# Performance work log

Measured on AMD Instinct MI355X. Metric: run time of the kernel, lower is better.

The kernel has to match this reference:

```python
import jax, jax.numpy as jnp
import numpy as np

N_NODES = 100000
N_EDGES = 1600000
HIDDEN = 128
N_LAYERS = 4
EPS = 0.0  # GINConv default eps, train_eps=False


def setup_inputs() -> dict:
    key = jax.random.key(0)
    ks = jax.random.split(key, 6)
    scale = 1.0 / np.sqrt(HIDDEN)
    return {
        "x": jax.random.normal(ks[0], (N_NODES, HIDDEN), dtype=jnp.float32),
        "edge_index": jax.random.randint(ks[1], (2, N_EDGES), 0, N_NODES, dtype=jnp.int64),
        "W1": jax.random.normal(ks[2], (N_LAYERS, HIDDEN, HIDDEN), dtype=jnp.float32) * scale,
        "b1": jnp.zeros((N_LAYERS, HIDDEN), dtype=jnp.float32),
        "W2": jax.random.normal(ks[3], (N_LAYERS, HIDDEN, HIDDEN), dtype=jnp.float32) * scale,
        "b2": jnp.zeros((N_LAYERS, HIDDEN), dtype=jnp.float32),
    }


def reference(x, edge_index, W1, b1, W2, b2):
    src = edge_index[0]  # message sources (x_j)
    dst = edge_index[1]  # aggregation targets
    n = x.shape[0]
    for l in range(N_LAYERS):
        x_in = x
        # scatter-add aggregation: sum_{j in N(i)} x_j
        agg = jax.ops.segment_sum(x[src], dst, num_segments=n)
        out = agg + (1.0 + EPS) * x
        # GIN MLP: Linear -> ReLU -> Linear
        h = jax.nn.relu(out @ W1[l] + b1[l]) @ W2[l] + b2[l]
        # outer loop: relu, dropout (identity in eval), residual
        x = x_in + jax.nn.relu(h)
    return x
```

## Files before the change

### kernel.cpp

```cpp
#include <hip/hip_runtime.h>

typedef unsigned short u16;
typedef unsigned int u32;

constexpr int NN = 100000;
constexpr int NE = 1600000;
constexpr int H = 128;

constexpr int NB = 196;
constexpr int BCAP = 10240;
constexpr int PB_E = 4096;
constexpr int PB_BLOCKS = (NE + PB_E - 1) / PB_E;

typedef __bf16 bf16x8 __attribute__((ext_vector_type(8)));
typedef float f32x16 __attribute__((ext_vector_type(16)));

__device__ __forceinline__ u16 f2bf(float f) {
    union { float f; u32 u; } cv; cv.f = f;
    u32 r = (cv.u + 0x7fffu + ((cv.u >> 16) & 1u)) >> 16;
    return (u16)r;
}
__device__ __forceinline__ float bflo(u32 u) {
    union { u32 u; float f; } cv; cv.u = u << 16; return cv.f;
}
__device__ __forceinline__ float bfhi(u32 u) {
    union { u32 u; float f; } cv; cv.u = u & 0xffff0000u; return cv.f;
}

__global__ void detect_kernel(const int* __restrict__ e, int* __restrict__ flag,
                              int* __restrict__ gcursor) {
    __shared__ int anynz;
    if (threadIdx.x == 0) anynz = 0;
    __syncthreads();
    int local = 0;
    for (int i = threadIdx.x; i < 4096; i += 256)
        if (e[2 * i + 1] != 0) local = 1;
    if (local) atomicOr(&anynz, 1);
    __syncthreads();
    if (threadIdx.x == 0) flag[0] = anynz ? 1 : 2;
    if (threadIdx.x < NB) gcursor[threadIdx.x] = 0;
}

__global__ __launch_bounds__(256) void part_kernel(const int* __restrict__ e,
                                                   const int* __restrict__ flag,
                                                   int* __restrict__ gcursor,
                                                   u32* __restrict__ ebuf) {
    __shared__ int lcnt[NB];
    __shared__ int gbaseL[NB];
    const int t = threadIdx.x;
    if (t < NB) lcnt[t] = 0;
    __syncthreads();
    const int st = flag[0];
    const int base = blockIdx.x * PB_E;
    u32 pk[16]; int bk[16]; int rk[16];
#pragma unroll
    for (int j = 0; j < 16; ++j) {
        int i = base + j * 256 + t;
        bk[j] = -1;
        if (i < NE) {
            int s = e[st * i];
            int d = e[st * (NE + i)];
            int b = d >> 9;
            pk[j] = (u32)s | ((u32)(d & 511) << 17);
            bk[j] = b;
            rk[j] = atomicAdd(&lcnt[b], 1);
        }
    }
    __syncthreads();
    if (t < NB) gbaseL[t] = atomicAdd(&gcursor[t], lcnt[t]);
    __syncthreads();
#pragma unroll
    for (int j = 0; j < 16; ++j)
        if (bk[j] >= 0)
            ebuf[bk[j] * BCAP + gbaseL[bk[j]] + rk[j]] = pk[j];
}

__global__ __launch_bounds__(256) void bscan_kernel(const int* __restrict__ gcursor,
                                                    int* __restrict__ bbase,
                                                    int* __restrict__ offs) {
    __shared__ int s[256];
    int t = threadIdx.x;
    int v = (t < NB) ? gcursor[t] : 0;
    s[t] = v;
    __syncthreads();
    for (int off = 1; off < 256; off <<= 1) {
        int u = (t >= off) ? s[t - off] : 0;
        __syncthreads();
        s[t] += u;
        __syncthreads();
    }
    if (t < NB) bbase[t] = s[t] - v;
    if (t == 0) offs[NN] = NE;
}

__global__ __launch_bounds__(256) void bfill_kernel(const u32* __restrict__ ebuf,
                                                    const int* __restrict__ gcursor,
                                                    const int* __restrict__ bbase,
                                                    int* __restrict__ offs,
                                                    int* __restrict__ colv) {
    __shared__ int ncnt[512];
    __shared__ int cur[512];
    __shared__ int ps[256];
    const int b = blockIdx.x, t = threadIdx.x;
    const int En = gcursor[b];
    const int bb = bbase[b];
    ncnt[t] = 0; ncnt[t + 256] = 0;
    __syncthreads();
    const u32* eb = ebuf + b * BCAP;
    for (int i = t; i < En; i += 256)
        atomicAdd(&ncnt[eb[i] >> 17], 1);
    __syncthreads();
    int s2 = ncnt[2 * t] + ncnt[2 * t + 1];
    ps[t] = s2;
    __syncthreads();
    for (int off = 1; off < 256; off <<= 1) {
        int u = (t >= off) ? ps[t - off] : 0;
        __syncthreads();
        ps[t] += u;
        __syncthreads();
    }
    int e0 = ps[t] - s2;
    cur[2 * t] = e0;
    cur[2 * t + 1] = e0 + ncnt[2 * t];
    __syncthreads();
    const int n0 = b * 512;
    for (int i = t; i < 512; i += 256)
        if (n0 + i < NN) offs[n0 + i] = bb + cur[i];
    __syncthreads();
    for (int i = t; i < En; i += 256) {
        u32 p = eb[i];
        int pos = atomicAdd(&cur[p >> 17], 1);
        colv[bb + pos] = (int)(p & 0x1FFFFu);
    }
}

__global__ void wtconv_kernel(const float* __restrict__ W1,
                              const float* __restrict__ W2,
                              u16* __restrict__ wt) {
    int t = blockIdx.x * 256 + threadIdx.x;
    int w = t >> 14;
    int r = t & 16383;
    int k = r >> 7, n = r & 127;
    int l = w >> 1, s = w & 1;
    const float* src = (s == 0 ? W1 : W2) + l * 16384;
    wt[w * 16384 + n * 128 + k] = f2bf(src[k * 128 + n]);
}

__global__ void xinit_kernel(const float* __restrict__ xin,
                             float* __restrict__ x, u16* __restrict__ xb) {
    int i = blockIdx.x * 256 + threadIdx.x;
    float4 v = ((const float4*)xin)[i];
    ((float4*)x)[i] = v;
    uint2 p;
    p.x = (u32)f2bf(v.x) | ((u32)f2bf(v.y) << 16);
    p.y = (u32)f2bf(v.z) | ((u32)f2bf(v.w) << 16);
    ((uint2*)xb)[i] = p;
}

__global__ __launch_bounds__(256) void agg_kernel(const u16* __restrict__ xb,
                                                  const int* __restrict__ colv,
                                                  const int* __restrict__ offs,
                                                  u16* __restrict__ out) {
    const int lane = threadIdx.x & 63;
    const int node = __builtin_amdgcn_readfirstlane(blockIdx.x * 4 + (threadIdx.x >> 6));
    const int rs = __builtin_amdgcn_readfirstlane(offs[node]);
    const int re = __builtin_amdgcn_readfirstlane(offs[node + 1]);
    u32 su = *(const u32*)(xb + node * H + lane * 2);
    float a0 = bflo(su), a1 = bfhi(su);
    for (int j = rs; j < re; j += 16) {
        int sidx[16];
#pragma unroll
        for (int q = 0; q < 16; ++q) {
            int idx = j + q;
            idx = idx < re ? idx : re - 1;
            sidx[q] = __builtin_amdgcn_readfirstlane(colv[idx]);
        }
        u32 uu[16];
#pragma unroll
        for (int q = 0; q < 16; ++q)
            uu[q] = *(const u32*)(xb + sidx[q] * H + lane * 2);
#pragma unroll
        for (int q = 0; q < 16; ++q) {
            u32 m = (j + q < re) ? 0xffffffffu : 0u;
            u32 u = uu[q] & m;
            a0 += bflo(u); a1 += bfhi(u);
        }
    }
    u32 o = (u32)f2bf(a0) | ((u32)f2bf(a1) << 16);
    *(u32*)(out + node * H + lane * 2) = o;
}

__global__ __launch_bounds__(256) void mlp_kernel(const u16* __restrict__ agg,
                                                  const u16* __restrict__ wt1,
                                                  const u16* __restrict__ wt2,
                                                  const float* __restrict__ b1,
                                                  const float* __restrict__ b2,
                                                  float* __restrict__ x,
                                                  u16* __restrict__ xb) {
    __shared__ u16 lds[128 * 128];
    const int tid = threadIdx.x;
    const int wave = tid >> 6, lane = tid & 63;
    const int wm = wave >> 1, wn = wave & 1;
    const int ml = lane & 31, g = lane >> 5;
    const int row0 = blockIdx.x * 128;

#pragma unroll
    for (int i = 0; i < 8; ++i) {
        int ch = tid + 256 * i;
        int r = ch >> 4, c = ch & 15;
        int4 v = make_int4(0, 0, 0, 0);
        int gr = row0 + r;
        if (gr < NN) v = *(const int4*)(agg + gr * H + c * 8);
        *(int4*)(&lds[r * H + ((c ^ (r & 15)) << 3)]) = v;
    }

    bf16x8 bfrag[2][8];
#pragma unroll
    for (int nt = 0; nt < 2; ++nt)
#pragma unroll
        for (int ks = 0; ks < 8; ++ks)
            bfrag[nt][ks] = *(const bf16x8*)(wt1 + (wn * 64 + nt * 32 + ml) * H + ks * 16 + g * 8);

    float bias1[2], bias2[2];
#pragma unroll
    for (int nt = 0; nt < 2; ++nt) {
        bias1[nt] = b1[wn * 64 + nt * 32 + ml];
        bias2[nt] = b2[wn * 64 + nt * 32 + ml];
    }

    __syncthreads();

    f32x16 acc[2][2];
#pragma unroll
    for (int mt = 0; mt < 2; ++mt)
#pragma unroll
        for (int nt = 0; nt < 2; ++nt)
#pragma unroll
            for (int i = 0; i < 16; ++i) acc[mt][nt][i] = 0.f;

#pragma unroll
    for (int ks = 0; ks < 8; ++ks) {
        bf16x8 afrag[2];
#pragma unroll
        for (int mt = 0; mt < 2; ++mt) {
            int m = wm * 64 + mt * 32 + ml;
            int chunk = (2 * ks + g) ^ (m & 15);
            afrag[mt] = *(const bf16x8*)(&lds[m * H + (chunk << 3)]);
        }
#pragma unroll
        for (int mt = 0; mt < 2; ++mt)
#pragma unroll
            for (int nt = 0; nt < 2; ++nt)
                acc[mt][nt] = __builtin_amdgcn_mfma_f32_32x32x16_bf16(
                    afrag[mt], bfrag[nt][ks], acc[mt][nt], 0, 0, 0);
    }

    __syncthreads();

#pragma unroll
    for (int mt = 0; mt < 2; ++mt)
#pragma unroll
        for (int nt = 0; nt < 2; ++nt)
#pragma unroll
            for (int reg = 0; reg < 16; ++reg) {
                int rm = wm * 64 + mt * 32 + (reg & 3) + ((reg >> 2) << 3) + 4 * g;
                int cn = wn * 64 + nt * 32 + ml;
                float v = acc[mt][nt][reg] + bias1[nt];
                v = v > 0.f ? v : 0.f;
                lds[rm * H + ((((cn >> 3) ^ (rm & 15))) << 3) + (cn & 7)] = f2bf(v);
            }

#pragma unroll
    for (int nt = 0; nt < 2; ++nt)
#pragma unroll
        for (int ks = 0; ks < 8; ++ks)
            bfrag[nt][ks] = *(const bf16x8*)(wt2 + (wn * 64 + nt * 32 + ml) * H + ks * 16 + g * 8);

#pragma unroll
    for (int mt = 0; mt < 2; ++mt)
#pragma unroll
        for (int nt = 0; nt < 2; ++nt)
#pragma unroll
            for (int i = 0; i < 16; ++i) acc[mt][nt][i] = 0.f;

    __syncthreads();

#pragma unroll
    for (int ks = 0; ks < 8; ++ks) {
        bf16x8 afrag[2];
#pragma unroll
        for (int mt = 0; mt < 2; ++mt) {
            int m = wm * 64 + mt * 32 + ml;
            int chunk = (2 * ks + g) ^ (m & 15);
            afrag[mt] = *(const bf16x8*)(&lds[m * H + (chunk << 3)]);
        }
#pragma unroll
        for (int mt = 0; mt < 2; ++mt)
#pragma unroll
            for (int nt = 0; nt < 2; ++nt)
                acc[mt][nt] = __builtin_amdgcn_mfma_f32_32x32x16_bf16(
                    afrag[mt], bfrag[nt][ks], acc[mt][nt], 0, 0, 0);
    }

    __syncthreads();

#pragma unroll
    for (int mt = 0; mt < 2; ++mt)
#pragma unroll
        for (int nt = 0; nt < 2; ++nt)
#pragma unroll
            for (int reg = 0; reg < 16; ++reg) {
                int rm = wm * 64 + mt * 32 + (reg & 3) + ((reg >> 2) << 3) + 4 * g;
                int cn = wn * 64 + nt * 32 + ml;
                float v = acc[mt][nt][reg] + bias2[nt];
                v = v > 0.f ? v : 0.f;
                lds[rm * H + ((((cn >> 3) ^ (rm & 15))) << 3) + (cn & 7)] = f2bf(v);
            }

    __syncthreads();

#pragma unroll
    for (int i = 0; i < 8; ++i) {
        int ch = tid + 256 * i;
        int r = ch >> 4, c = ch & 15;
        int gr = row0 + r;
        if (gr < NN) {
            int4 hv = *(const int4*)(&lds[r * H + ((c ^ (r & 15)) << 3)]);
            float4 x0 = *(const float4*)(x + gr * H + c * 8);
            float4 x1 = *(const float4*)(x + gr * H + c * 8 + 4);
            x0.x += bflo((u32)hv.x); x0.y += bfhi((u32)hv.x);
            x0.z += bflo((u32)hv.y); x0.w += bfhi((u32)hv.y);
            x1.x += bflo((u32)hv.z); x1.y += bfhi((u32)hv.z);
            x1.z += bflo((u32)hv.w); x1.w += bfhi((u32)hv.w);
            *(float4*)(x + gr * H + c * 8) = x0;
            *(float4*)(x + gr * H + c * 8 + 4) = x1;
            int4 xo;
            xo.x = (int)((u32)f2bf(x0.x) | ((u32)f2bf(x0.y) << 16));
            xo.y = (int)((u32)f2bf(x0.z) | ((u32)f2bf(x0.w) << 16));
            xo.z = (int)((u32)f2bf(x1.x) | ((u32)f2bf(x1.y) << 16));
            xo.w = (int)((u32)f2bf(x1.z) | ((u32)f2bf(x1.w) << 16));
            *(int4*)(xb + gr * H + c * 8) = xo;
        }
    }
}

extern "C" void kernel_launch(void* const* d_in, const int* in_sizes, int n_in,
                              void* d_out, int out_size, void* d_ws, size_t ws_size,
                              hipStream_t stream) {
    const float* x_in = (const float*)d_in[0];
    const int* edges = (const int*)d_in[1];
    const float* W1 = (const float*)d_in[2];
    const float* b1 = (const float*)d_in[3];
    const float* W2 = (const float*)d_in[4];
    const float* b2 = (const float*)d_in[5];
    float* x = (float*)d_out;

    char* ws = (char*)d_ws;
    int* flag = (int*)ws;
    int* gcursor = (int*)(ws + 512);
    int* bbase = (int*)(ws + 2048);
    int* offs = (int*)(ws + 4096);
    int* colv = (int*)(ws + 406528);
    u16* wt = (u16*)(ws + 6809600);
    u16* xb = (u16*)(ws + 7072768);
    u16* aggout = (u16*)(ws + 32672768);
    u32* ebuf = (u32*)aggout;

    detect_kernel<<<1, 256, 0, stream>>>(edges, flag, gcursor);
    part_kernel<<<PB_BLOCKS, 256, 0, stream>>>(edges, flag, gcursor, ebuf);
    bscan_kernel<<<1, 256, 0, stream>>>(gcursor, bbase, offs);
    bfill_kernel<<<NB, 256, 0, stream>>>(ebuf, gcursor, bbase, offs, colv);
    wtconv_kernel<<<131072 / 256, 256, 0, stream>>>(W1, W2, wt);
    xinit_kernel<<<(NN * H / 4) / 256, 256, 0, stream>>>(x_in, x, xb);

    for (int l = 0; l < 4; ++l) {
        agg_kernel<<<NN / 4, 256, 0, stream>>>(xb, colv, offs, aggout);
        mlp_kernel<<<(NN + 127) / 128, 256, 0, stream>>>(
            aggout, wt + (l * 2) * 16384, wt + (l * 2 + 1) * 16384,
            b1 + l * 128, b2 + l * 128, x, xb);
    }
}
```

Before: 556.1 us.

## Fuse neighbor aggregation into MLP kernel with ping-pong bf16 feature buffers

Removes the separate aggregation kernel and has each MLP block gather neighbor sums for its 128 rows directly into LDS, then runs the two GEMMs. This avoids writing and re-reading the aggregated bf16 tensor through global memory and saves a launch per layer. Because blocks now read features while others write updated ones, the bf16 feature copy is double-buffered across layers. The trade-off is far fewer waves doing the latency-bound gather serially, with a shallower unroll of in-flight loads.

```diff
diff --git a/kernel.cpp b/kernel.cpp
--- a/kernel.cpp
+++ b/kernel.cpp
@@ -157,46 +157,15 @@
     ((uint2*)xb)[i] = p;
 }
 
-__global__ __launch_bounds__(256) void agg_kernel(const u16* __restrict__ xb,
+__global__ __launch_bounds__(256) void mlp_kernel(const u16* __restrict__ xbin,
                                                   const int* __restrict__ colv,
                                                   const int* __restrict__ offs,
-                                                  u16* __restrict__ out) {
-    const int lane = threadIdx.x & 63;
-    const int node = __builtin_amdgcn_readfirstlane(blockIdx.x * 4 + (threadIdx.x >> 6));
-    const int rs = __builtin_amdgcn_readfirstlane(offs[node]);
-    const int re = __builtin_amdgcn_readfirstlane(offs[node + 1]);
-    u32 su = *(const u32*)(xb + node * H + lane * 2);
-    float a0 = bflo(su), a1 = bfhi(su);
-    for (int j = rs; j < re; j += 16) {
-        int sidx[16];
-#pragma unroll
-        for (int q = 0; q < 16; ++q) {
-            int idx = j + q;
-            idx = idx < re ? idx : re - 1;
-            sidx[q] = __builtin_amdgcn_readfirstlane(colv[idx]);
-        }
-        u32 uu[16];
-#pragma unroll
-        for (int q = 0; q < 16; ++q)
-            uu[q] = *(const u32*)(xb + sidx[q] * H + lane * 2);
-#pragma unroll
-        for (int q = 0; q < 16; ++q) {
-            u32 m = (j + q < re) ? 0xffffffffu : 0u;
-            u32 u = uu[q] & m;
-            a0 += bflo(u); a1 += bfhi(u);
-        }
-    }
-    u32 o = (u32)f2bf(a0) | ((u32)f2bf(a1) << 16);
-    *(u32*)(out + node * H + lane * 2) = o;
-}
-
-__global__ __launch_bounds__(256) void mlp_kernel(const u16* __restrict__ agg,
                                                   const u16* __restrict__ wt1,
                                                   const u16* __restrict__ wt2,
                                                   const float* __restrict__ b1,
                                                   const float* __restrict__ b2,
                                                   float* __restrict__ x,
-                                                  u16* __restrict__ xb) {
+                                                  u16* __restrict__ xbout) {
     __shared__ u16 lds[128 * 128];
     const int tid = threadIdx.x;
     const int wave = tid >> 6, lane = tid & 63;
@@ -204,14 +173,40 @@
     const int ml = lane & 31, g = lane >> 5;
     const int row0 = blockIdx.x * 128;
 
-#pragma unroll
-    for (int i = 0; i < 8; ++i) {
-        int ch = tid + 256 * i;
-        int r = ch >> 4, c = ch & 15;
-        int4 v = make_int4(0, 0, 0, 0);
-        int gr = row0 + r;
-        if (gr < NN) v = *(const int4*)(agg + gr * H + c * 8);
-        *(int4*)(&lds[r * H + ((c ^ (r & 15)) << 3)]) = v;
+    {
+        const int s0 = wave * 32;
+        for (int s = 0; s < 32; ++s) {
+            const int r = s0 + s;
+            const int node = row0 + r;
+            float a0 = 0.f, a1 = 0.f;
+            if (node < NN) {
+                const int rs = __builtin_amdgcn_readfirstlane(offs[node]);
+                const int re = __builtin_amdgcn_readfirstlane(offs[node + 1]);
+                u32 su = *(const u32*)(xbin + node * H + lane * 2);
+                a0 = bflo(su); a1 = bfhi(su);
+                for (int j = rs; j < re; j += 8) {
+                    int sidx[8];
+#pragma unroll
+                    for (int q = 0; q < 8; ++q) {
+                        int idx = j + q;
+                        idx = idx < re ? idx : re - 1;
+                        sidx[q] = __builtin_amdgcn_readfirstlane(colv[idx]);
+                    }
+                    u32 uu[8];
+#pragma unroll
+                    for (int q = 0; q < 8; ++q)
+                        uu[q] = *(const u32*)(xbin + sidx[q] * H + lane * 2);
+#pragma unroll
+                    for (int q = 0; q < 8; ++q) {
+                        u32 m = (j + q < re) ? 0xffffffffu : 0u;
+                        u32 u = uu[q] & m;
+                        a0 += bflo(u); a1 += bfhi(u);
+                    }
+                }
+            }
+            u32 o = (u32)f2bf(a0) | ((u32)f2bf(a1) << 16);
+            *(u32*)(&lds[r * H + (((lane >> 2) ^ (r & 15)) << 3) + ((lane & 3) << 1)]) = o;
+        }
     }
 
     bf16x8 bfrag[2][8];
@@ -339,7 +334,7 @@
             xo.y = (int)((u32)f2bf(x0.z) | ((u32)f2bf(x0.w) << 16));
             xo.z = (int)((u32)f2bf(x1.x) | ((u32)f2bf(x1.y) << 16));
             xo.w = (int)((u32)f2bf(x1.z) | ((u32)f2bf(x1.w) << 16));
-            *(int4*)(xb + gr * H + c * 8) = xo;
+            *(int4*)(xbout + gr * H + c * 8) = xo;
         }
     }
 }
@@ -362,21 +357,23 @@
     int* offs = (int*)(ws + 4096);
     int* colv = (int*)(ws + 406528);
     u16* wt = (u16*)(ws + 6809600);
-    u16* xb = (u16*)(ws + 7072768);
-    u16* aggout = (u16*)(ws + 32672768);
-    u32* ebuf = (u32*)aggout;
+    u16* xb0 = (u16*)(ws + 7072768);
+    u16* xb1 = (u16*)(ws + 32672768);
+    u32* ebuf = (u32*)xb1;
 
     detect_kernel<<<1, 256, 0, stream>>>(edges, flag, gcursor);
     part_kernel<<<PB_BLOCKS, 256, 0, stream>>>(edges, flag, gcursor, ebuf);
     bscan_kernel<<<1, 256, 0, stream>>>(gcursor, bbase, offs);
     bfill_kernel<<<NB, 256, 0, stream>>>(ebuf, gcursor, bbase, offs, colv);
     wtconv_kernel<<<131072 / 256, 256, 0, stream>>>(W1, W2, wt);
-    xinit_kernel<<<(NN * H / 4) / 256, 256, 0, stream>>>(x_in, x, xb);
+    xinit_kernel<<<(NN * H / 4) / 256, 256, 0, stream>>>(x_in, x, xb0);
 
     for (int l = 0; l < 4; ++l) {
-        agg_kernel<<<NN / 4, 256, 0, stream>>>(xb, colv, offs, aggout);
+        u16* xin = (l & 1) ? xb1 : xb0;
+        u16* xout = (l & 1) ? xb0 : xb1;
         mlp_kernel<<<(NN + 127) / 128, 256, 0, stream>>>(
-            aggout, wt + (l * 2) * 16384, wt + (l * 2 + 1) * 16384,
-            b1 + l * 128, b2 + l * 128, x, xb);
-    }
-}
+            xin, colv, offs,
+            wt + (l * 2) * 16384, wt + (l * 2 + 1) * 16384,
+            b1 + l * 128, b2 + l * 128, x, xout);
+    }
+}
```

Result: slower. 794.5 us (+42.9%).
